# Kernel tuning notes

Measured on AMD Instinct MI355X. Metric: run time of the kernel, lower is better.

The kernel has to match this reference:

```python
import jax, jax.numpy as jnp
import numpy as np

T = 8192   # sequence length (sent_len)
D = 512    # word_emb_dim
H = 2048   # enc_lstm_dim
S = 512    # number of segments (len(action_pos))
EPS = 1e-4 # additive constant in the original _masked_softmax denominator


def setup_inputs() -> dict:
    key = jax.random.key(0)
    ks = jax.random.split(key, 16)
    s = 0.02  # small init scale keeps exp() stable
    seg_len = T // S
    action_pos = (jnp.arange(1, S + 1, dtype=jnp.int32) * seg_len - 1)  # last = T-1
    action = jnp.zeros((T,), jnp.int32).at[action_pos].set(1)
    return {
        "sent": jax.random.normal(ks[0], (T, D), jnp.float32),
        "Wi1": jax.random.normal(ks[1], (3 * H, D), jnp.float32) * s,
        "Wh1": jax.random.normal(ks[2], (3 * H, H), jnp.float32) * s,
        "bi1": jax.random.normal(ks[3], (3 * H,), jnp.float32) * s,
        "bh1": jax.random.normal(ks[4], (3 * H,), jnp.float32) * s,
        "Wi2": jax.random.normal(ks[5], (3 * H, H), jnp.float32) * s,
        "Wh2": jax.random.normal(ks[6], (3 * H, H), jnp.float32) * s,
        "bi2": jax.random.normal(ks[7], (3 * H,), jnp.float32) * s,
        "bh2": jax.random.normal(ks[8], (3 * H,), jnp.float32) * s,
        "Wl": jax.random.normal(ks[9], (H, H), jnp.float32) * s,
        "bl": jax.random.normal(ks[10], (H,), jnp.float32) * s,
        "wa": jax.random.normal(ks[11], (H,), jnp.float32) * s,
        "Wl2": jax.random.normal(ks[12], (H, H), jnp.float32) * s,
        "bl2": jax.random.normal(ks[13], (H,), jnp.float32) * s,
        "wa2": jax.random.normal(ks[14], (H,), jnp.float32) * s,
        "action": action,
        "action_pos": action_pos,
    }


def _gru_scan(xs, reset, Wi, Wh, bi, bh):
    """GRU over leading axis; hidden state zeroed after steps where reset==1.
    xs: (N, in), reset: (N,) int. Returns outputs (N, H)."""
    gi_all = xs @ Wi.T + bi  # (N, 3H) precompute input gates as one GEMM

    def step(h, inp):
        gi, a = inp
        gh = Wh @ h + bh
        r = jax.nn.sigmoid(gi[:H] + gh[:H])
        z = jax.nn.sigmoid(gi[H:2 * H] + gh[H:2 * H])
        n = jnp.tanh(gi[2 * H:] + r * gh[2 * H:])
        hn = (1.0 - z) * n + z * h
        h_next = jnp.where(a == 1, jnp.zeros_like(hn), hn)
        return h_next, hn

    h0 = jnp.zeros((H,), xs.dtype)
    _, outs = jax.lax.scan(step, h0, (gi_all, reset))
    return outs


def _degenerate_softmax(a):
    # Original sums exp over a size-1 axis: w = exp(a) / (exp(a) + 1e-4)
    e = jnp.exp(a)
    return e / (e + EPS)


def reference(sent, Wi1, Wh1, bi1, bh1, Wi2, Wh2, bi2, bh2,
              Wl, bl, wa, Wl2, bl2, wa2, action, action_pos):
    # lower GRU with per-step state reset
    outs = _gru_scan(sent, action, Wi1, Wh1, bi1, bh1)          # (T, H)
    emb_h = jnp.tanh(outs @ Wl.T + bl)                           # (T, H)
    w = _degenerate_softmax(emb_h @ wa)                          # (T,)
    weighted = w[:, None] * emb_h                                # (T, H)
    # segment i covers tokens (action_pos[i-1], action_pos[i]]
    seg_id = jnp.searchsorted(action_pos, jnp.arange(T), side='left')
    seg = jax.ops.segment_max(weighted, seg_id, num_segments=S)  # (S, H)
    # upper GRU over segment embeddings (no resets, zero init)
    outs2 = _gru_scan(seg, jnp.zeros((S,), jnp.int32), Wi2, Wh2, bi2, bh2)
    e2 = jnp.tanh(outs2 @ Wl2.T + bl2)                           # (S, H)
    w2 = _degenerate_softmax(e2 @ wa2)                           # (S,)
    emb = jnp.max(w2[:, None] * e2, axis=0, keepdims=True)       # (1, H)
    return emb
```

## Files before the change

### kernel.cpp

```cpp
#include <hip/hip_runtime.h>
#include <stdint.h>

typedef unsigned short u16;
typedef unsigned int u32;
typedef unsigned long long u64;
typedef __attribute__((ext_vector_type(4))) float f32x4;
typedef __attribute__((ext_vector_type(8))) short bf16x8;
typedef __attribute__((ext_vector_type(4))) u32 u32x4;

constexpr int kT = 8192;
constexpr int kD = 512;
constexpr int kH = 2048;
constexpr int kH3 = 6144;
constexpr int kS = 512;
constexpr int kSeg = 16;
constexpr int kNWG2 = 256;
constexpr int kREP = 4;

__device__ __forceinline__ float bf2f(u16 u) {
  union { float f; u32 u; } v; v.u = ((u32)u) << 16; return v.f;
}
__device__ __forceinline__ u16 f2bf(float f) {
  union { float f; u32 u; } v; v.f = f;
  u32 lsb = (v.u >> 16) & 1u;
  v.u += 0x7fffu + lsb;
  return (u16)(v.u >> 16);
}
__device__ __forceinline__ float bflo(u32 x) {
  union { float f; u32 u; } v; v.u = x << 16; return v.f;
}
__device__ __forceinline__ float bfhi(u32 x) {
  union { float f; u32 u; } v; v.u = x & 0xffff0000u; return v.f;
}
__device__ __forceinline__ float sigm(float x) { return 1.f / (1.f + expf(-x)); }

__device__ __forceinline__ void g2l16(const u16* g, u16* l) {
  __builtin_amdgcn_global_load_lds(
      (const __attribute__((address_space(1))) u32*)g,
      (__attribute__((address_space(3))) u32*)l, 16, 0, 0);
}

__device__ __forceinline__ u32x4 bypass_load16(const u32* p) {
  u32x4 v;
  asm volatile("global_load_dwordx4 %0, %1, off sc0 sc1\n\ts_waitcnt vmcnt(0)"
               : "=&v"(v) : "v"(p) : "memory");
  return v;
}
__device__ __forceinline__ void bypass_store16(u32* p, u32x4 v) {
  asm volatile("global_store_dwordx4 %0, %1, off sc0 sc1" :: "v"(p), "v"(v) : "memory");
}

__global__ void cvt_bf16(const float* __restrict__ in, u16* __restrict__ out, int n4) {
  int i = blockIdx.x * blockDim.x + threadIdx.x;
  if (i >= n4) return;
  const float4 v = *(const float4*)(in + (size_t)i * 4);
  uint2 o;
  o.x = (u32)f2bf(v.x) | ((u32)f2bf(v.y) << 16);
  o.y = (u32)f2bf(v.z) | ((u32)f2bf(v.w) << 16);
  *(uint2*)(out + (size_t)i * 4) = o;
}

template<int EPI>
__global__ __launch_bounds__(256)
void gemm_bt(const u16* __restrict__ A, int lda,
             const u16* __restrict__ B, int ldb,
             u16* __restrict__ Obf, const float* __restrict__ bias,
             int M, int N, int K)
{
  __shared__ u16 ls[4 * 16384];
  const int tid = threadIdx.x;
  const int w = tid >> 6, lane = tid & 63;
  const int wr = w >> 1, wc = w & 1;
  const int arow0 = blockIdx.y * 128;
  const int brow0 = blockIdx.x * 128;
  const int srow = w * 32 + (lane >> 3);
  const int scol = (lane & 7) * 8;
  const u16* gA = A + (size_t)(arow0 + srow) * lda + scol;
  const u16* gB = B + (size_t)(brow0 + srow) * ldb + scol;
  const int sb = w * 32 * 64;

  f32x4 acc[4][4];
#pragma unroll
  for (int m = 0; m < 4; ++m)
#pragma unroll
    for (int n = 0; n < 4; ++n) acc[m][n] = (f32x4)0.f;

  const int fr = lane & 15;
  const int kq = lane >> 4;
  const int nk = K >> 6;

  auto stage = [&](int buf, int kt) {
    u16* la = &ls[buf * 16384 + sb];
    u16* lb = &ls[buf * 16384 + 8192 + sb];
#pragma unroll
    for (int i = 0; i < 4; ++i) g2l16(gA + (size_t)i * 8 * lda + kt, la + i * 8 * 64);
#pragma unroll
    for (int i = 0; i < 4; ++i) g2l16(gB + (size_t)i * 8 * ldb + kt, lb + i * 8 * 64);
  };

  stage(0, 0);
  if (nk > 1) stage(1, 64);
  if (nk > 2) stage(2, 128);

  for (int i = 0; i < nk; ++i) {
    if (i + 2 < nk) asm volatile("s_waitcnt vmcnt(16)" ::: "memory");
    else            asm volatile("s_waitcnt vmcnt(0)" ::: "memory");
    __builtin_amdgcn_s_barrier();
    __builtin_amdgcn_sched_barrier(0);
    if (i + 3 < nk) stage((i + 3) & 3, (i + 3) * 64);
    const u16* lsA = &ls[(i & 3) * 16384];
    const u16* lsB = lsA + 8192;
#pragma unroll
    for (int kk = 0; kk < 2; ++kk) {
      bf16x8 af[4], bq[4];
#pragma unroll
      for (int m = 0; m < 4; ++m)
        af[m] = *(const bf16x8*)&lsA[(wr * 64 + m * 16 + fr) * 64 + kk * 32 + kq * 8];
#pragma unroll
      for (int n = 0; n < 4; ++n)
        bq[n] = *(const bf16x8*)&lsB[(wc * 64 + n * 16 + fr) * 64 + kk * 32 + kq * 8];
#pragma unroll
      for (int m = 0; m < 4; ++m)
#pragma unroll
        for (int n = 0; n < 4; ++n)
          acc[m][n] = __builtin_amdgcn_mfma_f32_16x16x32_bf16(af[m], bq[n], acc[m][n], 0, 0, 0);
    }
  }

#pragma unroll
  for (int m = 0; m < 4; ++m) {
#pragma unroll
    for (int n = 0; n < 4; ++n) {
      const int row0 = arow0 + wr * 64 + m * 16 + kq * 4;
      const int col = brow0 + wc * 64 + n * 16 + fr;
      if (EPI == 1) {
#pragma unroll
        for (int i = 0; i < 4; ++i)
          Obf[(size_t)(row0 + i) * N + col] = f2bf(acc[m][n][i]);
      } else {
        const float bv = bias[col];
#pragma unroll
        for (int i = 0; i < 4; ++i)
          Obf[(size_t)(row0 + i) * N + col] = f2bf(tanhf(acc[m][n][i] + bv));
      }
    }
  }
}

__global__ __launch_bounds__(256) void gru1_gates(
    const u32* __restrict__ gi32, int segStride, const u16* __restrict__ gh,
    const float* __restrict__ bi, const float* __restrict__ bh,
    u16* __restrict__ h_bf, u16* __restrict__ outs_bf, int t)
{
  const int idx = blockIdx.x * 256 + threadIdx.x;
  const int seg = idx >> 10, jp = idx & 1023;
  const u32* gh32 = (const u32*)gh;
  const int gbase = seg * segStride;
  const int base = seg * 3072;
  const u32 gir = gi32[gbase + jp],        ghr = gh32[base + jp];
  const u32 giz = gi32[gbase + 1024 + jp], ghz = gh32[base + 1024 + jp];
  const u32 gin = gi32[gbase + 2048 + jp], ghn = gh32[base + 2048 + jp];
  const float2 bir = *(const float2*)&bi[2 * jp];
  const float2 biz = *(const float2*)&bi[kH + 2 * jp];
  const float2 bin = *(const float2*)&bi[2 * kH + 2 * jp];
  const float2 bhr = *(const float2*)&bh[2 * jp];
  const float2 bhz = *(const float2*)&bh[kH + 2 * jp];
  const float2 bhn = *(const float2*)&bh[2 * kH + 2 * jp];
  const u32 hp = ((const u32*)h_bf)[seg * 1024 + jp];
  float hn[2];
#pragma unroll
  for (int e = 0; e < 2; ++e) {
    const float gr = e ? bfhi(gir) : bflo(gir), hr = e ? bfhi(ghr) : bflo(ghr);
    const float gz = e ? bfhi(giz) : bflo(giz), hz = e ? bfhi(ghz) : bflo(ghz);
    const float gn = e ? bfhi(gin) : bflo(gin), hh = e ? bfhi(ghn) : bflo(ghn);
    const float r = sigm(gr + (e ? bir.y : bir.x) + hr + (e ? bhr.y : bhr.x));
    const float z = sigm(gz + (e ? biz.y : biz.x) + hz + (e ? bhz.y : bhz.x));
    const float n = tanhf(gn + (e ? bin.y : bin.x) + r * (hh + (e ? bhn.y : bhn.x)));
    const float hprev = e ? bfhi(hp) : bflo(hp);
    hn[e] = (1.f - z) * n + z * hprev;
  }
  const u32 packed = (u32)f2bf(hn[0]) | ((u32)f2bf(hn[1]) << 16);
  ((u32*)h_bf)[seg * 1024 + jp] = packed;
  ((u32*)outs_bf)[(size_t)(seg * kSeg + t) * 1024 + jp] = packed;
}

__global__ __launch_bounds__(256) void seg_weight_max(
    const u16* __restrict__ embh, const float* __restrict__ wa,
    u16* __restrict__ seg_bf)
{
  __shared__ float wrow[16];
  const int s = blockIdx.x, tid = threadIdx.x;
  const int w = tid >> 6, lane = tid & 63;
#pragma unroll
  for (int rr = 0; rr < 4; ++rr) {
    const int r = w * 4 + rr;
    const u16* row = embh + ((size_t)s * kSeg + r) * kH;
    float p = 0.f;
#pragma unroll
    for (int k = 0; k < 32; ++k) {
      const int c = lane + 64 * k;
      p += bf2f(row[c]) * wa[c];
    }
#pragma unroll
    for (int off = 32; off; off >>= 1) p += __shfl_down(p, off, 64);
    if (lane == 0) { const float e = expf(p); wrow[r] = e / (e + 1e-4f); }
  }
  __syncthreads();
#pragma unroll
  for (int i = 0; i < 8; ++i) {
    const int c = tid + 256 * i;
    float m = -1e30f;
#pragma unroll
    for (int r = 0; r < 16; ++r)
      m = fmaxf(m, wrow[r] * bf2f(embh[((size_t)s * kSeg + r) * kH + c]));
    seg_bf[(size_t)s * kH + c] = f2bf(m);
  }
}

__global__ __launch_bounds__(512)
void gru2_persistent(const u16* __restrict__ Wh2bf, const u16* __restrict__ gi2b,
                     const float* __restrict__ bi2, const float* __restrict__ bh2,
                     u32* __restrict__ hx,
                     u16* __restrict__ outs2)
{
  __shared__ u16 wl[24 * kH];
  __shared__ u32 hlb[1024];
  __shared__ float gil_all[512 * 24];
  __shared__ float rowsum[24];
  __shared__ alignas(16) u16 hnl[8];
  const int wg = blockIdx.x, tid = threadIdx.x;
  const int g0 = wg * 8;
  const int rep = wg & (kREP - 1);
  uint4* wl4 = (uint4*)wl;
  for (int i = tid; i < 24 * 256; i += 512) {
    const int lr = i >> 8, q = i & 255;
    const int grow = (lr >> 3) * kH + g0 + (lr & 7);
    wl4[i] = ((const uint4*)Wh2bf)[(size_t)grow * 256 + q];
  }
  for (int i = tid; i < 512 * 24; i += 512) {
    const int t = i / 24, idx = i - t * 24;
    gil_all[i] = bf2f(gi2b[(size_t)t * kH3 + (idx >> 3) * kH + g0 + (idx & 7)]);
  }
  float bir = 0, biz = 0, bin = 0, bhr = 0, bhz = 0, bhn = 0;
  if (tid < 8) {
    const int jj = g0 + tid;
    bir = bi2[jj]; biz = bi2[kH + jj]; bin = bi2[2 * kH + jj];
    bhr = bh2[jj]; bhz = bh2[kH + jj]; bhn = bh2[2 * kH + jj];
  }
  const int w = tid >> 6, lane = tid & 63;
  const uint4* hl4 = (const uint4*)hlb;

  for (int t = 0; t < 512; ++t) {
    const u32 want = (u32)t & 0xffffu;
    const u32* p = hx + ((size_t)(t & 1) * kREP + rep) * 2048 + 4 * tid;
    u32x4 v = bypass_load16(p);
    for (;;) {
      const u32 bad = ((v.x ^ want) | (v.y ^ want) | (v.z ^ want) | (v.w ^ want)) & 0xffffu;
      if (!__any((int)bad)) break;
      if (bad) {
        __builtin_amdgcn_s_sleep(2);
        v = bypass_load16(p);
      }
    }
    hlb[2 * tid]     = (v.x >> 16) | (v.y & 0xffff0000u);
    hlb[2 * tid + 1] = (v.z >> 16) | (v.w & 0xffff0000u);
    __syncthreads();
#pragma unroll
    for (int rr = 0; rr < 3; ++rr) {
      const int lr = w * 3 + rr;
      float p2 = 0.f;
#pragma unroll
      for (int k = 0; k < 4; ++k) {
        const int q = lane + 64 * k;
        const uint4 wv = wl4[lr * 256 + q];
        const uint4 hv = hl4[q];
        p2 += bflo(wv.x) * bflo(hv.x) + bfhi(wv.x) * bfhi(hv.x);
        p2 += bflo(wv.y) * bflo(hv.y) + bfhi(wv.y) * bfhi(hv.y);
        p2 += bflo(wv.z) * bflo(hv.z) + bfhi(wv.z) * bfhi(hv.z);
        p2 += bflo(wv.w) * bflo(hv.w) + bfhi(wv.w) * bfhi(hv.w);
      }
#pragma unroll
      for (int off = 32; off; off >>= 1) p2 += __shfl_down(p2, off, 64);
      if (lane == 0) rowsum[lr] = p2;
    }
    __syncthreads();
    if (tid < 8) {
      const float r = sigm(gil_all[t * 24 + tid] + bir + rowsum[tid] + bhr);
      const float z = sigm(gil_all[t * 24 + 8 + tid] + biz + rowsum[8 + tid] + bhz);
      const float n = tanhf(gil_all[t * 24 + 16 + tid] + bin +
                            r * (rowsum[16 + tid] + bhn));
      const u32 hw = hlb[(g0 + tid) >> 1];
      const float hprev = (tid & 1) ? bfhi(hw) : bflo(hw);
      hnl[tid] = f2bf((1.f - z) * n + z * hprev);
    }
    __syncthreads();
    if (tid < 2 * kREP) {
      const int orep = tid >> 1, half = tid & 1;
      const u16* h4 = hnl + half * 4;
      const u32 tagv = (u32)(t + 1) & 0xffffu;
      u32x4 m;
      m.x = ((u32)h4[0] << 16) | tagv;
      m.y = ((u32)h4[1] << 16) | tagv;
      m.z = ((u32)h4[2] << 16) | tagv;
      m.w = ((u32)h4[3] << 16) | tagv;
      u32* q = hx + ((size_t)((t + 1) & 1) * kREP + orep) * 2048 + wg * 8 + half * 4;
      bypass_store16(q, m);
    }
    if (tid == 0)
      *(uint4*)&outs2[(size_t)t * kH + g0] = *(const uint4*)hnl;
  }
}

__global__ void calc_w2(const u16* __restrict__ e2, const float* __restrict__ wa2,
                        float* __restrict__ w2) {
  const int s = blockIdx.x, lane = threadIdx.x;
  float p = 0.f;
#pragma unroll
  for (int k = 0; k < 32; ++k) {
    const int c = lane + 64 * k;
    p += bf2f(e2[(size_t)s * kH + c]) * wa2[c];
  }
#pragma unroll
  for (int off = 32; off; off >>= 1) p += __shfl_down(p, off, 64);
  if (lane == 0) { const float e = expf(p); w2[s] = e / (e + 1e-4f); }
}

__global__ void final_max(const u16* __restrict__ e2, const float* __restrict__ w2,
                          float* __restrict__ out) {
  const int j = blockIdx.x * blockDim.x + threadIdx.x;
  float m = -1e30f;
  for (int s = 0; s < 512; ++s)
    m = fmaxf(m, w2[s] * bf2f(e2[(size_t)s * kH + j]));
  out[j] = m;
}

extern "C" void kernel_launch(void* const* d_in, const int* in_sizes, int n_in,
                              void* d_out, int out_size, void* d_ws, size_t ws_size,
                              hipStream_t stream)
{
  (void)in_sizes; (void)n_in; (void)out_size;
  const float* sent = (const float*)d_in[0];
  const float* Wi1f = (const float*)d_in[1];
  const float* Wh1f = (const float*)d_in[2];
  const float* bi1  = (const float*)d_in[3];
  const float* bh1  = (const float*)d_in[4];
  const float* Wi2f = (const float*)d_in[5];
  const float* Wh2f = (const float*)d_in[6];
  const float* bi2  = (const float*)d_in[7];
  const float* bh2  = (const float*)d_in[8];
  const float* Wlf  = (const float*)d_in[9];
  const float* bl   = (const float*)d_in[10];
  const float* wa   = (const float*)d_in[11];
  const float* Wl2f = (const float*)d_in[12];
  const float* bl2  = (const float*)d_in[13];
  const float* wa2  = (const float*)d_in[14];
  float* out = (float*)d_out;

  char* base = (char*)d_ws;
  size_t off = 0;
  auto alloc = [&](size_t b) { char* p = base + off; off += (b + 255) & ~(size_t)255; return p; };
  u16* sent_bf = (u16*)alloc((size_t)kT * kD * 2);
  u16* Wi1b    = (u16*)alloc((size_t)kH3 * kD * 2);
  u16* Wh1b    = (u16*)alloc((size_t)kH3 * kH * 2);
  u16* Wi2b    = (u16*)alloc((size_t)kH3 * kH * 2);
  u16* Wh2b    = (u16*)alloc((size_t)kH3 * kH * 2);
  u16* Wlb     = (u16*)alloc((size_t)kH * kH * 2);
  u16* Wl2b    = (u16*)alloc((size_t)kH * kH * 2);
  u16* gi_buf  = (u16*)alloc((size_t)kS * kH3 * 2);
  u16* gh_buf  = (u16*)alloc((size_t)kS * kH3 * 2);
  u16* h1b     = (u16*)alloc((size_t)kS * kH * 2);
  u16* outs_bf = (u16*)alloc((size_t)kT * kH * 2);
  u16* seg_bf  = (u16*)alloc((size_t)kS * kH * 2);
  u32* hx      = (u32*)alloc((size_t)2 * kREP * 2048 * 4);
  u16* outs2   = (u16*)alloc((size_t)kS * kH * 2);
  u16* e2b     = (u16*)alloc((size_t)kS * kH * 2);
  float* w2    = (float*)alloc(kS * 4);
  const size_t off_before_gi = off;
  u16* gi_all  = (u16*)alloc((size_t)kT * kH3 * 2);
  const bool fused_gi = (off <= ws_size);
  if (!fused_gi) off = off_before_gi;
  u16* embh = sent_bf;
  u16* gi2b = gi_buf;

  (void)hipMemsetAsync(h1b, 0, (size_t)kS * kH * 2, stream);
  (void)hipMemsetAsync(hx, 0, (size_t)2 * kREP * 2048 * 4, stream);

  auto cvt = [&](const float* src, u16* dst, int n) {
    const int n4 = n / 4;
    cvt_bf16<<<dim3((n4 + 255) / 256), dim3(256), 0, stream>>>(src, dst, n4);
  };
  cvt(sent, sent_bf, kT * kD);
  cvt(Wi1f, Wi1b, kH3 * kD);
  cvt(Wh1f, Wh1b, kH3 * kH);
  cvt(Wi2f, Wi2b, kH3 * kH);
  cvt(Wlf, Wlb, kH * kH);
  cvt(Wl2f, Wl2b, kH * kH);
  cvt(Wh2f, Wh2b, kH3 * kH);

  if (fused_gi) {
    gemm_bt<1><<<dim3(kH3 / 128, kT / 128), dim3(256), 0, stream>>>(
        sent_bf, kD, Wi1b, kD, gi_all, nullptr, kT, kH3, kD);
  }
  for (int t = 0; t < kSeg; ++t) {
    gemm_bt<1><<<dim3(kH3 / 128, kS / 128), dim3(256), 0, stream>>>(
        h1b, kH, Wh1b, kH, gh_buf, nullptr, kS, kH3, kH);
    const u32* gi32;
    int segStride;
    if (fused_gi) {
      gi32 = (const u32*)gi_all + (size_t)t * 3072;
      segStride = kSeg * 3072;
    } else {
      gemm_bt<1><<<dim3(kH3 / 128, kS / 128), dim3(256), 0, stream>>>(
          sent_bf + t * kD, kSeg * kD, Wi1b, kD, gi_buf, nullptr, kS, kH3, kD);
      gi32 = (const u32*)gi_buf;
      segStride = 3072;
    }
    gru1_gates<<<dim3(kS * kH / 512), dim3(256), 0, stream>>>(
        gi32, segStride, gh_buf, bi1, bh1, h1b, outs_bf, t);
  }
  gemm_bt<2><<<dim3(kH / 128, kT / 128), dim3(256), 0, stream>>>(
      outs_bf, kH, Wlb, kH, embh, bl, kT, kH, kH);
  seg_weight_max<<<dim3(kS), dim3(256), 0, stream>>>(embh, wa, seg_bf);
  gemm_bt<1><<<dim3(kH3 / 128, kS / 128), dim3(256), 0, stream>>>(
      seg_bf, kH, Wi2b, kH, gi2b, nullptr, kS, kH3, kH);
  gru2_persistent<<<dim3(kNWG2), dim3(512), 0, stream>>>(
      Wh2b, gi2b, bi2, bh2, hx, outs2);
  gemm_bt<2><<<dim3(kH / 128, kS / 128), dim3(256), 0, stream>>>(
      outs2, kH, Wl2b, kH, e2b, bl2, kS, kH, kH);
  calc_w2<<<dim3(kS), dim3(64), 0, stream>>>(e2b, wa2, w2);
  final_max<<<dim3(kH / 256), dim3(256), 0, stream>>>(e2b, w2, out);
}
```

Before: 2.972 ms.

## Keep GRU2 recurrent weights in registers and skip first-step Wh1 GEMM

The persistent upper-GRU kernel now holds each wave's three weight-row slices in registers instead of shared memory, and reads h into per-lane float arrays. The double-buffered h in shared memory lets it drop one barrier per step, and the spin-wait no longer sleeps. The lower GRU skips the recurrent GEMM and the h memset on the first step of each segment, where the hidden state is zero. Risks are higher register pressure, harder polling of the memory system without the sleep, and a possible race on hnl now that the barrier is gone.

```diff
diff --git a/kernel.cpp b/kernel.cpp
--- a/kernel.cpp
+++ b/kernel.cpp
@@ -150,23 +150,29 @@
 __global__ __launch_bounds__(256) void gru1_gates(
     const u32* __restrict__ gi32, int segStride, const u16* __restrict__ gh,
     const float* __restrict__ bi, const float* __restrict__ bh,
-    u16* __restrict__ h_bf, u16* __restrict__ outs_bf, int t)
+    u16* __restrict__ h_bf, u16* __restrict__ outs_bf, int t, int ghvalid)
 {
   const int idx = blockIdx.x * 256 + threadIdx.x;
   const int seg = idx >> 10, jp = idx & 1023;
   const u32* gh32 = (const u32*)gh;
   const int gbase = seg * segStride;
   const int base = seg * 3072;
-  const u32 gir = gi32[gbase + jp],        ghr = gh32[base + jp];
-  const u32 giz = gi32[gbase + 1024 + jp], ghz = gh32[base + 1024 + jp];
-  const u32 gin = gi32[gbase + 2048 + jp], ghn = gh32[base + 2048 + jp];
+  const u32 gir = gi32[gbase + jp];
+  const u32 giz = gi32[gbase + 1024 + jp];
+  const u32 gin = gi32[gbase + 2048 + jp];
+  u32 ghr = 0, ghz = 0, ghn = 0, hp = 0;
+  if (ghvalid) {
+    ghr = gh32[base + jp];
+    ghz = gh32[base + 1024 + jp];
+    ghn = gh32[base + 2048 + jp];
+    hp = ((const u32*)h_bf)[seg * 1024 + jp];
+  }
   const float2 bir = *(const float2*)&bi[2 * jp];
   const float2 biz = *(const float2*)&bi[kH + 2 * jp];
   const float2 bin = *(const float2*)&bi[2 * kH + 2 * jp];
   const float2 bhr = *(const float2*)&bh[2 * jp];
   const float2 bhz = *(const float2*)&bh[kH + 2 * jp];
   const float2 bhn = *(const float2*)&bh[2 * kH + 2 * jp];
-  const u32 hp = ((const u32*)h_bf)[seg * 1024 + jp];
   float hn[2];
 #pragma unroll
   for (int e = 0; e < 2; ++e) {
@@ -223,19 +229,28 @@
                      u32* __restrict__ hx,
                      u16* __restrict__ outs2)
 {
-  __shared__ u16 wl[24 * kH];
-  __shared__ u32 hlb[1024];
+  __shared__ u32 hlb[2][1024];
   __shared__ float gil_all[512 * 24];
   __shared__ float rowsum[24];
-  __shared__ alignas(16) u16 hnl[8];
+  __shared__ u16 hnl[8];
   const int wg = blockIdx.x, tid = threadIdx.x;
   const int g0 = wg * 8;
   const int rep = wg & (kREP - 1);
-  uint4* wl4 = (uint4*)wl;
-  for (int i = tid; i < 24 * 256; i += 512) {
-    const int lr = i >> 8, q = i & 255;
+  const int w = tid >> 6, lane = tid & 63;
+
+  u32 w0[16], w1[16], w2r[16];
+#pragma unroll
+  for (int rr = 0; rr < 3; ++rr) {
+    const int lr = w * 3 + rr;
     const int grow = (lr >> 3) * kH + g0 + (lr & 7);
-    wl4[i] = ((const uint4*)Wh2bf)[(size_t)grow * 256 + q];
+    const u32* src = (const u32*)(Wh2bf + (size_t)grow * kH) + lane * 16;
+#pragma unroll
+    for (int i = 0; i < 16; ++i) {
+      const u32 val = src[i];
+      if (rr == 0) w0[i] = val;
+      else if (rr == 1) w1[i] = val;
+      else w2r[i] = val;
+    }
   }
   for (int i = tid; i < 512 * 24; i += 512) {
     const int t = i / 24, idx = i - t * 24;
@@ -247,41 +262,47 @@
     bir = bi2[jj]; biz = bi2[kH + jj]; bin = bi2[2 * kH + jj];
     bhr = bh2[jj]; bhz = bh2[kH + jj]; bhn = bh2[2 * kH + jj];
   }
-  const int w = tid >> 6, lane = tid & 63;
-  const uint4* hl4 = (const uint4*)hlb;
 
   for (int t = 0; t < 512; ++t) {
+    const int par = t & 1;
     const u32 want = (u32)t & 0xffffu;
-    const u32* p = hx + ((size_t)(t & 1) * kREP + rep) * 2048 + 4 * tid;
+    const u32* p = hx + ((size_t)par * kREP + rep) * 2048 + 4 * tid;
     u32x4 v = bypass_load16(p);
     for (;;) {
       const u32 bad = ((v.x ^ want) | (v.y ^ want) | (v.z ^ want) | (v.w ^ want)) & 0xffffu;
       if (!__any((int)bad)) break;
-      if (bad) {
-        __builtin_amdgcn_s_sleep(2);
-        v = bypass_load16(p);
-      }
-    }
-    hlb[2 * tid]     = (v.x >> 16) | (v.y & 0xffff0000u);
-    hlb[2 * tid + 1] = (v.z >> 16) | (v.w & 0xffff0000u);
+      if (bad) v = bypass_load16(p);
+    }
+    hlb[par][2 * tid]     = (v.x >> 16) | (v.y & 0xffff0000u);
+    hlb[par][2 * tid + 1] = (v.z >> 16) | (v.w & 0xffff0000u);
     __syncthreads();
-#pragma unroll
-    for (int rr = 0; rr < 3; ++rr) {
-      const int lr = w * 3 + rr;
-      float p2 = 0.f;
-#pragma unroll
-      for (int k = 0; k < 4; ++k) {
-        const int q = lane + 64 * k;
-        const uint4 wv = wl4[lr * 256 + q];
-        const uint4 hv = hl4[q];
-        p2 += bflo(wv.x) * bflo(hv.x) + bfhi(wv.x) * bfhi(hv.x);
-        p2 += bflo(wv.y) * bflo(hv.y) + bfhi(wv.y) * bfhi(hv.y);
-        p2 += bflo(wv.z) * bflo(hv.z) + bfhi(wv.z) * bfhi(hv.z);
-        p2 += bflo(wv.w) * bflo(hv.w) + bfhi(wv.w) * bfhi(hv.w);
-      }
-#pragma unroll
-      for (int off = 32; off; off >>= 1) p2 += __shfl_down(p2, off, 64);
-      if (lane == 0) rowsum[lr] = p2;
+    const uint4* hp4 = (const uint4*)&hlb[par][0];
+    float hf[32];
+#pragma unroll
+    for (int q = 0; q < 4; ++q) {
+      const uint4 hv = hp4[lane * 4 + q];
+      hf[8 * q + 0] = bflo(hv.x); hf[8 * q + 1] = bfhi(hv.x);
+      hf[8 * q + 2] = bflo(hv.y); hf[8 * q + 3] = bfhi(hv.y);
+      hf[8 * q + 4] = bflo(hv.z); hf[8 * q + 5] = bfhi(hv.z);
+      hf[8 * q + 6] = bflo(hv.w); hf[8 * q + 7] = bfhi(hv.w);
+    }
+    float a0 = 0.f, a1 = 0.f, a2 = 0.f;
+#pragma unroll
+    for (int i = 0; i < 16; ++i) {
+      a0 += bflo(w0[i]) * hf[2 * i] + bfhi(w0[i]) * hf[2 * i + 1];
+      a1 += bflo(w1[i]) * hf[2 * i] + bfhi(w1[i]) * hf[2 * i + 1];
+      a2 += bflo(w2r[i]) * hf[2 * i] + bfhi(w2r[i]) * hf[2 * i + 1];
+    }
+#pragma unroll
+    for (int off = 32; off; off >>= 1) {
+      a0 += __shfl_down(a0, off, 64);
+      a1 += __shfl_down(a1, off, 64);
+      a2 += __shfl_down(a2, off, 64);
+    }
+    if (lane == 0) {
+      rowsum[w * 3 + 0] = a0;
+      rowsum[w * 3 + 1] = a1;
+      rowsum[w * 3 + 2] = a2;
     }
     __syncthreads();
     if (tid < 8) {
@@ -289,21 +310,19 @@
       const float z = sigm(gil_all[t * 24 + 8 + tid] + biz + rowsum[8 + tid] + bhz);
       const float n = tanhf(gil_all[t * 24 + 16 + tid] + bin +
                             r * (rowsum[16 + tid] + bhn));
-      const u32 hw = hlb[(g0 + tid) >> 1];
+      const u32 hw = hlb[par][(g0 + tid) >> 1];
       const float hprev = (tid & 1) ? bfhi(hw) : bflo(hw);
       hnl[tid] = f2bf((1.f - z) * n + z * hprev);
     }
-    __syncthreads();
     if (tid < 2 * kREP) {
       const int orep = tid >> 1, half = tid & 1;
-      const u16* h4 = hnl + half * 4;
       const u32 tagv = (u32)(t + 1) & 0xffffu;
       u32x4 m;
-      m.x = ((u32)h4[0] << 16) | tagv;
-      m.y = ((u32)h4[1] << 16) | tagv;
-      m.z = ((u32)h4[2] << 16) | tagv;
-      m.w = ((u32)h4[3] << 16) | tagv;
-      u32* q = hx + ((size_t)((t + 1) & 1) * kREP + orep) * 2048 + wg * 8 + half * 4;
+      m.x = ((u32)hnl[half * 4 + 0] << 16) | tagv;
+      m.y = ((u32)hnl[half * 4 + 1] << 16) | tagv;
+      m.z = ((u32)hnl[half * 4 + 2] << 16) | tagv;
+      m.w = ((u32)hnl[half * 4 + 3] << 16) | tagv;
+      u32* q = hx + ((size_t)(1 - par) * kREP + orep) * 2048 + wg * 8 + half * 4;
       bypass_store16(q, m);
     }
     if (tid == 0)
@@ -382,7 +401,6 @@
   u16* embh = sent_bf;
   u16* gi2b = gi_buf;
 
-  (void)hipMemsetAsync(h1b, 0, (size_t)kS * kH * 2, stream);
   (void)hipMemsetAsync(hx, 0, (size_t)2 * kREP * 2048 * 4, stream);
 
   auto cvt = [&](const float* src, u16* dst, int n) {
@@ -402,8 +420,10 @@
         sent_bf, kD, Wi1b, kD, gi_all, nullptr, kT, kH3, kD);
   }
   for (int t = 0; t < kSeg; ++t) {
-    gemm_bt<1><<<dim3(kH3 / 128, kS / 128), dim3(256), 0, stream>>>(
-        h1b, kH, Wh1b, kH, gh_buf, nullptr, kS, kH3, kH);
+    if (t > 0) {
+      gemm_bt<1><<<dim3(kH3 / 128, kS / 128), dim3(256), 0, stream>>>(
+          h1b, kH, Wh1b, kH, gh_buf, nullptr, kS, kH3, kH);
+    }
     const u32* gi32;
     int segStride;
     if (fused_gi) {
@@ -416,7 +436,7 @@
       segStride = 3072;
     }
     gru1_gates<<<dim3(kS * kH / 512), dim3(256), 0, stream>>>(
-        gi32, segStride, gh_buf, bi1, bh1, h1b, outs_bf, t);
+        gi32, segStride, gh_buf, bi1, bh1, h1b, outs_bf, t, t > 0 ? 1 : 0);
   }
   gemm_bt<2><<<dim3(kH / 128, kT / 128), dim3(256), 0, stream>>>(
       outs_bf, kH, Wlb, kH, embh, bl, kT, kH, kH);
```

Result: faster. 2.510 ms (-15.5%).
